# Performance work log

Hardware: AMD Instinct MI355X
Metric: run time of the kernel (lower is better)

## Reference

```python
import jax, jax.numpy as jnp
import numpy as np

N_NODES = 100000
N_EDGES = 3200000
IN_DIM = 128
OUT_DIM = 128


def setup_inputs() -> dict:
    key = jax.random.key(0)
    k1, k2, k3, k4, k5 = jax.random.split(key, 5)
    fea_input = jax.random.normal(k1, (N_NODES, IN_DIM), dtype=jnp.float32)
    edge_row = jax.random.randint(k2, (N_EDGES,), 0, N_NODES, dtype=jnp.int32)
    edge_col = jax.random.randint(k3, (N_EDGES,), 0, N_NODES, dtype=jnp.int32)
    edge_val = jax.random.uniform(k4, (N_EDGES,), dtype=jnp.float32)
    # kaiming_uniform-style init for weight, zeros for bias
    bound = float(np.sqrt(6.0 / IN_DIM))
    weight = jax.random.uniform(k5, (IN_DIM, OUT_DIM), dtype=jnp.float32,
                                minval=-bound, maxval=bound)
    bias = jnp.zeros((OUT_DIM,), dtype=jnp.float32)
    return {
        "fea_input": fea_input,
        "edge_row": edge_row,
        "edge_col": edge_col,
        "edge_val": edge_val,
        "weight": weight,
        "bias": bias,
    }


def reference(fea_input, edge_row, edge_col, edge_val, weight, bias):
    # support = X @ W  -> [N, OUT_DIM]
    support = jnp.matmul(fea_input, weight)
    # SpMM: out[r] += val * support[c] for each edge (r, c, val)
    gathered = support[edge_col] * edge_val[:, None]  # [E, OUT_DIM]
    output = jax.ops.segment_sum(gathered, edge_row, num_segments=N_NODES)
    return output + bias
```

## Files before the change

kernel.cpp:

```cpp
#include <hip/hip_runtime.h>
#include <hip/hip_bf16.h>


#define N_NODES 100000
#define N_EDGES 3200000
#define DIM 128
#define RB 16
#define RPB 64
#define NBKT ((N_NODES + RPB - 1) / RPB)
#define CHUNK 8192
#define NCHK ((N_EDGES + CHUNK - 1) / CHUNK)
#define CAP3 2688

typedef __attribute__((ext_vector_type(8))) short bf16x8;
typedef __attribute__((ext_vector_type(4))) float f32x4;
typedef unsigned long long u64;
typedef unsigned int u32;

__device__ inline ushort bf16rne(float f) {
  uint32_t u = __float_as_uint(f);
  u += 0x7fffu + ((u >> 16) & 1u);
  return (ushort)(u >> 16);
}
__device__ inline float lofl(u32 u) { return __uint_as_float(u << 16); }
__device__ inline float hifl(u32 u) { return __uint_as_float(u & 0xffff0000u); }

__global__ __launch_bounds__(256) void prep_count_kernel(
    const float* __restrict__ X, const float* __restrict__ W,
    ushort* __restrict__ Xh, ushort* __restrict__ Wh,
    const int* __restrict__ erow, int* __restrict__ bcnt,
    int* __restrict__ table) {
  __shared__ int cnt[NBKT];
  if (blockIdx.x < 1024) {
    const size_t nx4 = (size_t)N_NODES * DIM / 4;
    const size_t nw4 = (size_t)DIM * DIM / 4;
    for (size_t i = (size_t)blockIdx.x * blockDim.x + threadIdx.x;
         i < nx4 + nw4; i += (size_t)1024 * blockDim.x) {
      const float4 f = (i < nx4) ? ((const float4*)X)[i] : ((const float4*)W)[i - nx4];
      ushort4 h;
      h.x = bf16rne(f.x); h.y = bf16rne(f.y); h.z = bf16rne(f.z); h.w = bf16rne(f.w);
      if (i < nx4) ((ushort4*)Xh)[i] = h;
      else         ((ushort4*)Wh)[i - nx4] = h;
    }
  } else {
    const int cb = blockIdx.x - 1024;
    for (int b = threadIdx.x; b < NBKT; b += 256) cnt[b] = 0;
    __syncthreads();
    const int e0 = cb * CHUNK;
    #pragma unroll
    for (int it = 0; it < CHUNK / 256; ++it) {
      const int e = e0 + it * 256 + threadIdx.x;
      if (e < N_EDGES) atomicAdd(&cnt[erow[e] >> 6], 1);
    }
    __syncthreads();
    for (int b = threadIdx.x; b < NBKT; b += 256) {
      const int c = cnt[b];
      table[(size_t)cb * NBKT + b] = c;
      if (c) atomicAdd(&bcnt[b], c);
    }
  }
}

__global__ __launch_bounds__(1024) void bscan_kernel(int* __restrict__ bcur,
                                                     int* __restrict__ bbase) {
  __shared__ int wsum[32];
  const int t = threadIdx.x, lane = t & 63, wid = t >> 6;
  int v0 = (t < NBKT) ? bcur[t] : 0;
  int v1 = (t + 1024 < NBKT) ? bcur[t + 1024] : 0;
  int i0 = v0, i1 = v1;
  #pragma unroll
  for (int off = 1; off < 64; off <<= 1) {
    int n0 = __shfl_up(i0, off, 64);
    int n1 = __shfl_up(i1, off, 64);
    if (lane >= off) { i0 += n0; i1 += n1; }
  }
  if (lane == 63) { wsum[wid] = i0; wsum[16 + wid] = i1; }
  __syncthreads();
  if (t == 0) {
    int s = 0;
    #pragma unroll
    for (int k = 0; k < 32; ++k) { int x = wsum[k]; wsum[k] = s; s += x; }
    bbase[NBKT] = s;
  }
  __syncthreads();
  const int e0 = wsum[wid] + i0 - v0;
  const int e1 = wsum[16 + wid] + i1 - v1;
  if (t < NBKT) { bbase[t] = e0; bcur[t] = e0; }
  if (t + 1024 < NBKT) { bbase[t + 1024] = e1; bcur[t + 1024] = e1; }
}

__global__ __launch_bounds__(256) void partition_kernel(
    const int* __restrict__ erow, const int* __restrict__ ecol,
    const float* __restrict__ eval, const int* __restrict__ table,
    int* __restrict__ bcur, u64* __restrict__ p64) {
  __shared__ int cnt[NBKT];
  const int e0 = blockIdx.x * CHUNK;
  for (int b = threadIdx.x; b < NBKT; b += 256) {
    const int c = table[(size_t)blockIdx.x * NBKT + b];
    cnt[b] = c ? atomicAdd(&bcur[b], c) : 0;
  }
  __syncthreads();
  #pragma unroll
  for (int it = 0; it < CHUNK / 256; ++it) {
    const int e = e0 + it * 256 + threadIdx.x;
    if (e < N_EDGES) {
      const int r = erow[e];
      const u32 lo = ((u32)ecol[e] << 15) | (u32)bf16rne(eval[e]);
      const int p = atomicAdd(&cnt[r >> 6], 1);
      p64[p] = ((u64)(r & (RPB - 1)) << 32) | (u64)lo;
    }
  }
}

__global__ __launch_bounds__(256) void agg_sort_kernel(
    const ushort* __restrict__ Xh,
    const int* __restrict__ bbase, const u64* __restrict__ p64,
    ushort* __restrict__ Yh) {
  __shared__ u32 sbuf[CAP3];
  __shared__ int hist[RPB];
  __shared__ int rstart[RPB];
  __shared__ int curs[RPB];
  const int b = blockIdx.x, t = threadIdx.x;
  const int s = bbase[b];
  int nE = bbase[b + 1] - s;
  if (nE > CAP3) nE = CAP3;

  if (t < RPB) hist[t] = 0;
  __syncthreads();
  for (int i = t; i < nE; i += 256)
    atomicAdd(&hist[(int)(p64[s + i] >> 32) & (RPB - 1)], 1);
  __syncthreads();
  if (t < RPB) {
    const int v = hist[t];
    int incl = v;
    #pragma unroll
    for (int off = 1; off < 64; off <<= 1) {
      int n = __shfl_up(incl, off, 64);
      if (t >= off) incl += n;
    }
    rstart[t] = incl - v;
    curs[t] = incl - v;
  }
  __syncthreads();
  for (int i = t; i < nE; i += 256) {
    const u64 w = p64[s + i];
    const int p = atomicAdd(&curs[(int)(w >> 32) & (RPB - 1)], 1);
    sbuf[p] = (u32)w;
  }
  __syncthreads();

  const int wid = t >> 6, lane = t & 63;
  const int q = lane >> 4;
  const u32 sub16 = (u32)(lane & 15) * 16u;
  const char* Xb = (const char*)Xh;
  #pragma unroll 1
  for (int j = 0; j < 16; ++j) {
    const int rl = wid * 16 + j;
    const int gr = b * RPB + rl;
    const int s0 = rstart[rl];
    const int s1 = s0 + hist[rl];
    float f0 = 0.f, f1 = 0.f, f2 = 0.f, f3 = 0.f;
    float f4 = 0.f, f5 = 0.f, f6 = 0.f, f7 = 0.f;
    #pragma unroll 1
    for (int e = s0 + q; e < s1; e += 16) {
      const u32 lo0 = sbuf[e];
      const u32 lo1 = (e + 4  < s1) ? sbuf[e + 4]  : 0u;
      const u32 lo2 = (e + 8  < s1) ? sbuf[e + 8]  : 0u;
      const u32 lo3 = (e + 12 < s1) ? sbuf[e + 12] : 0u;
      const u32 o0 = (lo0 >> 7) & 0xFFFFFF00u;
      const u32 o1 = (lo1 >> 7) & 0xFFFFFF00u;
      const u32 o2 = (lo2 >> 7) & 0xFFFFFF00u;
      const u32 o3 = (lo3 >> 7) & 0xFFFFFF00u;
      const uint4 g0 = *(const uint4*)(Xb + (o0 + sub16));
      const uint4 g1 = *(const uint4*)(Xb + (o1 + sub16));
      const uint4 g2 = *(const uint4*)(Xb + (o2 + sub16));
      const uint4 g3 = *(const uint4*)(Xb + (o3 + sub16));
      const float v0 = __uint_as_float((lo0 & 0x7fffu) << 16);
      const float v1 = __uint_as_float((lo1 & 0x7fffu) << 16);
      const float v2 = __uint_as_float((lo2 & 0x7fffu) << 16);
      const float v3 = __uint_as_float((lo3 & 0x7fffu) << 16);
      f0 += v0 * lofl(g0.x); f1 += v0 * hifl(g0.x);
      f2 += v0 * lofl(g0.y); f3 += v0 * hifl(g0.y);
      f4 += v0 * lofl(g0.z); f5 += v0 * hifl(g0.z);
      f6 += v0 * lofl(g0.w); f7 += v0 * hifl(g0.w);
      f0 += v1 * lofl(g1.x); f1 += v1 * hifl(g1.x);
      f2 += v1 * lofl(g1.y); f3 += v1 * hifl(g1.y);
      f4 += v1 * lofl(g1.z); f5 += v1 * hifl(g1.z);
      f6 += v1 * lofl(g1.w); f7 += v1 * hifl(g1.w);
      f0 += v2 * lofl(g2.x); f1 += v2 * hifl(g2.x);
      f2 += v2 * lofl(g2.y); f3 += v2 * hifl(g2.y);
      f4 += v2 * lofl(g2.z); f5 += v2 * hifl(g2.z);
      f6 += v2 * lofl(g2.w); f7 += v2 * hifl(g2.w);
      f0 += v3 * lofl(g3.x); f1 += v3 * hifl(g3.x);
      f2 += v3 * lofl(g3.y); f3 += v3 * hifl(g3.y);
      f4 += v3 * lofl(g3.z); f5 += v3 * hifl(g3.z);
      f6 += v3 * lofl(g3.w); f7 += v3 * hifl(g3.w);
    }
    f0 += __shfl_xor(f0, 16); f1 += __shfl_xor(f1, 16);
    f2 += __shfl_xor(f2, 16); f3 += __shfl_xor(f3, 16);
    f4 += __shfl_xor(f4, 16); f5 += __shfl_xor(f5, 16);
    f6 += __shfl_xor(f6, 16); f7 += __shfl_xor(f7, 16);
    f0 += __shfl_xor(f0, 32); f1 += __shfl_xor(f1, 32);
    f2 += __shfl_xor(f2, 32); f3 += __shfl_xor(f3, 32);
    f4 += __shfl_xor(f4, 32); f5 += __shfl_xor(f5, 32);
    f6 += __shfl_xor(f6, 32); f7 += __shfl_xor(f7, 32);
    if (gr < N_NODES && lane < 16) {
      uint4 o;
      o.x = (u32)bf16rne(f0) | ((u32)bf16rne(f1) << 16);
      o.y = (u32)bf16rne(f2) | ((u32)bf16rne(f3) << 16);
      o.z = (u32)bf16rne(f4) | ((u32)bf16rne(f5) << 16);
      o.w = (u32)bf16rne(f6) | ((u32)bf16rne(f7) << 16);
      ((uint4*)(Yh + (size_t)gr * DIM))[lane] = o;
    }
  }
}

__global__ __launch_bounds__(256) void gemm_mfma(const ushort* __restrict__ Yh,
                                                 const ushort* __restrict__ Wh,
                                                 const float* __restrict__ bias,
                                                 float* __restrict__ out) {
  const int wid = threadIdx.x >> 6, lane = threadIdx.x & 63;
  const int lr = lane & 15, lq = lane >> 4;
  const int n0 = wid * 32;

  bf16x8 bfrag[4][2];
  float bval[2];
  #pragma unroll
  for (int nt = 0; nt < 2; ++nt) {
    const int col = n0 + nt * 16 + lr;
    bval[nt] = bias[col];
    #pragma unroll
    for (int kk = 0; kk < 4; ++kk) {
      const int kbase = kk * 32 + lq * 8;
      bf16x8 b;
      #pragma unroll
      for (int i = 0; i < 8; ++i)
        b[i] = (short)Wh[(size_t)(kbase + i) * DIM + col];
      bfrag[kk][nt] = b;
    }
  }

  const int r0 = blockIdx.x * 256;
  #pragma unroll 1
  for (int g = 0; g < 16; ++g) {
    const int m0 = r0 + g * 16;
    if (m0 >= N_NODES) break;
    bf16x8 afrag[4];
    const ushort* arow = Yh + (size_t)(m0 + lr) * DIM + lq * 8;
    #pragma unroll
    for (int kk = 0; kk < 4; ++kk)
      afrag[kk] = *(const bf16x8*)(arow + kk * 32);
    #pragma unroll
    for (int nt = 0; nt < 2; ++nt) {
      f32x4 acc = {0.f, 0.f, 0.f, 0.f};
      #pragma unroll
      for (int kk = 0; kk < 4; ++kk)
        acc = __builtin_amdgcn_mfma_f32_16x16x32_bf16(afrag[kk], bfrag[kk][nt], acc, 0, 0, 0);
      const int col = n0 + nt * 16 + lr;
      #pragma unroll
      for (int j = 0; j < 4; ++j)
        out[(size_t)(m0 + lq * 4 + j) * DIM + col] = acc[j] + bval[nt];
    }
  }
}

__global__ __launch_bounds__(128) void gemm_kernel(
    const float* __restrict__ IN, const float* __restrict__ W,
    float* __restrict__ OUT, const float* __restrict__ bias, int add_bias) {
  __shared__ float Wsh[DIM * DIM];
  __shared__ float Xsh[RB * DIM];
  const int t = threadIdx.x;
  #pragma unroll 8
  for (int i = 0; i < DIM; ++i) Wsh[i * DIM + t] = W[i * DIM + t];
  const int r0 = blockIdx.x * RB;
  #pragma unroll
  for (int idx = t; idx < RB * DIM; idx += 128)
    Xsh[idx] = IN[(size_t)r0 * DIM + idx];
  __syncthreads();
  float acc[RB];
  const float b = add_bias ? bias[t] : 0.f;
  #pragma unroll
  for (int r = 0; r < RB; ++r) acc[r] = b;
  for (int k = 0; k < DIM; ++k) {
    const float w = Wsh[k * DIM + t];
    #pragma unroll
    for (int r = 0; r < RB; ++r) acc[r] += Xsh[r * DIM + k] * w;
  }
  #pragma unroll
  for (int r = 0; r < RB; ++r)
    OUT[(size_t)(r0 + r) * DIM + t] = acc[r];
}

__global__ void init_kernel(float* __restrict__ out, const float* __restrict__ bias) {
  const size_t total4 = (size_t)N_NODES * DIM / 4;
  const float4* b4 = (const float4*)bias;
  float4* o4 = (float4*)out;
  for (size_t i = (size_t)blockIdx.x * blockDim.x + threadIdx.x;
       i < total4; i += (size_t)gridDim.x * blockDim.x)
    o4[i] = b4[i & 31];
}

__global__ __launch_bounds__(256) void scatter_kernel(
    const float* __restrict__ S,
    const int* __restrict__ erow, const int* __restrict__ ecol,
    const float* __restrict__ eval, float* __restrict__ out) {
  const long long g = (long long)blockIdx.x * blockDim.x + threadIdx.x;
  const long long e = g >> 5;
  const int lane = (int)(g & 31);
  if (e >= N_EDGES) return;
  const int r = erow[e];
  const int c = ecol[e];
  const float v = eval[e];
  const float4 x = ((const float4*)(S + (size_t)c * DIM))[lane];
  float* o = out + (size_t)r * DIM + lane * 4;
  atomicAdd(o + 0, v * x.x);
  atomicAdd(o + 1, v * x.y);
  atomicAdd(o + 2, v * x.z);
  atomicAdd(o + 3, v * x.w);
}

extern "C" void kernel_launch(void* const* d_in, const int* in_sizes, int n_in,
                              void* d_out, int out_size, void* d_ws, size_t ws_size,
                              hipStream_t stream) {
  const float* X    = (const float*)d_in[0];
  const int*   erow = (const int*)d_in[1];
  const int*   ecol = (const int*)d_in[2];
  const float* eval = (const float*)d_in[3];
  const float* W    = (const float*)d_in[4];
  const float* bias = (const float*)d_in[5];
  float* out = (float*)d_out;

  const size_t P64_BYTES = (size_t)N_EDGES * 8;
  const size_t XH_BYTES  = (size_t)N_NODES * DIM * 2;
  const size_t YH_BYTES  = (size_t)N_NODES * DIM * 2;
  const size_t WH_BYTES  = (size_t)DIM * DIM * 2;
  const size_t BB_BYTES  = (size_t)(NBKT + 1) * 4;
  const size_t BC_BYTES  = (size_t)NBKT * 4;
  const size_t NEED = P64_BYTES + XH_BYTES + YH_BYTES + WH_BYTES +
                      BB_BYTES + BC_BYTES + 256;

  if (ws_size >= NEED) {
    char* w = (char*)d_ws;
    u64*    p64     = (u64*)w;     w += P64_BYTES;
    ushort* Xh      = (ushort*)w;  w += XH_BYTES;
    ushort* Yh      = (ushort*)w;  w += YH_BYTES;
    ushort* Wh      = (ushort*)w;  w += WH_BYTES;
    int*    bbase   = (int*)w;     w += BB_BYTES;
    int*    bcur    = (int*)w;
    int*    table   = (int*)Yh;

    hipMemsetAsync(bcur, 0, BC_BYTES, stream);
    prep_count_kernel<<<1024 + NCHK, 256, 0, stream>>>(X, W, Xh, Wh, erow, bcur, table);
    bscan_kernel<<<1, 1024, 0, stream>>>(bcur, bbase);
    partition_kernel<<<NCHK, 256, 0, stream>>>(erow, ecol, eval, table, bcur, p64);
    agg_sort_kernel<<<NBKT, 256, 0, stream>>>(Xh, bbase, p64, Yh);
    gemm_mfma<<<(N_NODES + 255) / 256, 256, 0, stream>>>(Yh, Wh, bias, out);
  } else {
    float* S = (float*)d_ws;
    init_kernel<<<2048, 256, 0, stream>>>(out, bias);
    gemm_kernel<<<N_NODES / RB, 128, 0, stream>>>(X, W, S, bias, 0);
    const long long threads = (long long)N_EDGES * 32;
    scatter_kernel<<<(int)((threads + 255) / 256), 256, 0, stream>>>(S, erow, ecol, eval, out);
  }
}
```

Measured before the change: 232.4 us.

## Replace atomic bucket offsets with per-bucket chunk prefix scan; pre-transpose W

Bucket offsets are no longer claimed with global atomics. Per-chunk histograms are exclusive-scanned per bucket in a new column-scan kernel, so each partition block gets deterministic write offsets, and the memset goes away. Separately, W is stored transposed in bf16 so the GEMM loads each B fragment with one vector load instead of eight strided scalar loads. The cost is an extra kernel launch and a strided scan over the table, where each lane reads a value NBKT ints apart.

```diff
diff --git a/kernel.cpp b/kernel.cpp
--- a/kernel.cpp
+++ b/kernel.cpp
@@ -27,20 +27,28 @@
 
 __global__ __launch_bounds__(256) void prep_count_kernel(
     const float* __restrict__ X, const float* __restrict__ W,
-    ushort* __restrict__ Xh, ushort* __restrict__ Wh,
-    const int* __restrict__ erow, int* __restrict__ bcnt,
-    int* __restrict__ table) {
+    ushort* __restrict__ Xh, ushort* __restrict__ WhT,
+    const int* __restrict__ erow, int* __restrict__ table) {
   __shared__ int cnt[NBKT];
   if (blockIdx.x < 1024) {
     const size_t nx4 = (size_t)N_NODES * DIM / 4;
     const size_t nw4 = (size_t)DIM * DIM / 4;
     for (size_t i = (size_t)blockIdx.x * blockDim.x + threadIdx.x;
          i < nx4 + nw4; i += (size_t)1024 * blockDim.x) {
-      const float4 f = (i < nx4) ? ((const float4*)X)[i] : ((const float4*)W)[i - nx4];
-      ushort4 h;
-      h.x = bf16rne(f.x); h.y = bf16rne(f.y); h.z = bf16rne(f.z); h.w = bf16rne(f.w);
-      if (i < nx4) ((ushort4*)Xh)[i] = h;
-      else         ((ushort4*)Wh)[i - nx4] = h;
+      if (i < nx4) {
+        const float4 f = ((const float4*)X)[i];
+        ushort4 h;
+        h.x = bf16rne(f.x); h.y = bf16rne(f.y); h.z = bf16rne(f.z); h.w = bf16rne(f.w);
+        ((ushort4*)Xh)[i] = h;
+      } else {
+        const float4 f = ((const float4*)W)[i - nx4];
+        const int elem = (int)(i - nx4) * 4;
+        const int k = elem >> 7, col = elem & 127;
+        WhT[(size_t)(col + 0) * DIM + k] = bf16rne(f.x);
+        WhT[(size_t)(col + 1) * DIM + k] = bf16rne(f.y);
+        WhT[(size_t)(col + 2) * DIM + k] = bf16rne(f.z);
+        WhT[(size_t)(col + 3) * DIM + k] = bf16rne(f.w);
+      }
     }
   } else {
     const int cb = blockIdx.x - 1024;
@@ -53,20 +61,39 @@
       if (e < N_EDGES) atomicAdd(&cnt[erow[e] >> 6], 1);
     }
     __syncthreads();
-    for (int b = threadIdx.x; b < NBKT; b += 256) {
-      const int c = cnt[b];
-      table[(size_t)cb * NBKT + b] = c;
-      if (c) atomicAdd(&bcnt[b], c);
-    }
-  }
-}
-
-__global__ __launch_bounds__(1024) void bscan_kernel(int* __restrict__ bcur,
+    for (int b = threadIdx.x; b < NBKT; b += 256)
+      table[(size_t)cb * NBKT + b] = cnt[b];
+  }
+}
+
+__global__ __launch_bounds__(256) void cscan_kernel(int* __restrict__ table,
+                                                    int* __restrict__ bcnt) {
+  const int b = blockIdx.x * 4 + (threadIdx.x >> 6);
+  if (b >= NBKT) return;
+  const int lane = threadIdx.x & 63;
+  int carry = 0;
+  #pragma unroll
+  for (int r = 0; r < (NCHK + 63) / 64; ++r) {
+    const int cb = r * 64 + lane;
+    const int c = (cb < NCHK) ? table[(size_t)cb * NBKT + b] : 0;
+    int incl = c;
+    #pragma unroll
+    for (int off = 1; off < 64; off <<= 1) {
+      int n = __shfl_up(incl, off, 64);
+      if (lane >= off) incl += n;
+    }
+    if (cb < NCHK) table[(size_t)cb * NBKT + b] = carry + incl - c;
+    carry += __shfl(incl, 63, 64);
+  }
+  if (lane == 0) bcnt[b] = carry;
+}
+
+__global__ __launch_bounds__(1024) void bscan_kernel(const int* __restrict__ bcnt,
                                                      int* __restrict__ bbase) {
   __shared__ int wsum[32];
   const int t = threadIdx.x, lane = t & 63, wid = t >> 6;
-  int v0 = (t < NBKT) ? bcur[t] : 0;
-  int v1 = (t + 1024 < NBKT) ? bcur[t + 1024] : 0;
+  int v0 = (t < NBKT) ? bcnt[t] : 0;
+  int v1 = (t + 1024 < NBKT) ? bcnt[t + 1024] : 0;
   int i0 = v0, i1 = v1;
   #pragma unroll
   for (int off = 1; off < 64; off <<= 1) {
@@ -83,22 +110,18 @@
     bbase[NBKT] = s;
   }
   __syncthreads();
-  const int e0 = wsum[wid] + i0 - v0;
-  const int e1 = wsum[16 + wid] + i1 - v1;
-  if (t < NBKT) { bbase[t] = e0; bcur[t] = e0; }
-  if (t + 1024 < NBKT) { bbase[t + 1024] = e1; bcur[t + 1024] = e1; }
+  if (t < NBKT) bbase[t] = wsum[wid] + i0 - v0;
+  if (t + 1024 < NBKT) bbase[t + 1024] = wsum[16 + wid] + i1 - v1;
 }
 
 __global__ __launch_bounds__(256) void partition_kernel(
     const int* __restrict__ erow, const int* __restrict__ ecol,
     const float* __restrict__ eval, const int* __restrict__ table,
-    int* __restrict__ bcur, u64* __restrict__ p64) {
+    const int* __restrict__ bbase, u64* __restrict__ p64) {
   __shared__ int cnt[NBKT];
   const int e0 = blockIdx.x * CHUNK;
-  for (int b = threadIdx.x; b < NBKT; b += 256) {
-    const int c = table[(size_t)blockIdx.x * NBKT + b];
-    cnt[b] = c ? atomicAdd(&bcur[b], c) : 0;
-  }
+  for (int b = threadIdx.x; b < NBKT; b += 256)
+    cnt[b] = bbase[b] + table[(size_t)blockIdx.x * NBKT + b];
   __syncthreads();
   #pragma unroll
   for (int it = 0; it < CHUNK / 256; ++it) {
@@ -216,7 +239,7 @@
 }
 
 __global__ __launch_bounds__(256) void gemm_mfma(const ushort* __restrict__ Yh,
-                                                 const ushort* __restrict__ Wh,
+                                                 const ushort* __restrict__ WhT,
                                                  const float* __restrict__ bias,
                                                  float* __restrict__ out) {
   const int wid = threadIdx.x >> 6, lane = threadIdx.x & 63;
@@ -230,14 +253,8 @@
     const int col = n0 + nt * 16 + lr;
     bval[nt] = bias[col];
     #pragma unroll
-    for (int kk = 0; kk < 4; ++kk) {
-      const int kbase = kk * 32 + lq * 8;
-      bf16x8 b;
-      #pragma unroll
-      for (int i = 0; i < 8; ++i)
-        b[i] = (short)Wh[(size_t)(kbase + i) * DIM + col];
-      bfrag[kk][nt] = b;
-    }
+    for (int kk = 0; kk < 4; ++kk)
+      bfrag[kk][nt] = *(const bf16x8*)(WhT + (size_t)col * DIM + kk * 32 + lq * 8);
   }
 
   const int r0 = blockIdx.x * 256;
@@ -333,10 +350,10 @@
   const size_t P64_BYTES = (size_t)N_EDGES * 8;
   const size_t XH_BYTES  = (size_t)N_NODES * DIM * 2;
   const size_t YH_BYTES  = (size_t)N_NODES * DIM * 2;
-  const size_t WH_BYTES  = (size_t)DIM * DIM * 2;
+  const size_t WHT_BYTES = (size_t)DIM * DIM * 2;
   const size_t BB_BYTES  = (size_t)(NBKT + 1) * 4;
   const size_t BC_BYTES  = (size_t)NBKT * 4;
-  const size_t NEED = P64_BYTES + XH_BYTES + YH_BYTES + WH_BYTES +
+  const size_t NEED = P64_BYTES + XH_BYTES + YH_BYTES + WHT_BYTES +
                       BB_BYTES + BC_BYTES + 256;
 
   if (ws_size >= NEED) {
@@ -344,17 +361,17 @@
     u64*    p64     = (u64*)w;     w += P64_BYTES;
     ushort* Xh      = (ushort*)w;  w += XH_BYTES;
     ushort* Yh      = (ushort*)w;  w += YH_BYTES;
-    ushort* Wh      = (ushort*)w;  w += WH_BYTES;
+    ushort* WhT     = (ushort*)w;  w += WHT_BYTES;
     int*    bbase   = (int*)w;     w += BB_BYTES;
-    int*    bcur    = (int*)w;
+    int*    bcnt    = (int*)w;     w += BC_BYTES;
     int*    table   = (int*)Yh;
 
-    hipMemsetAsync(bcur, 0, BC_BYTES, stream);
-    prep_count_kernel<<<1024 + NCHK, 256, 0, stream>>>(X, W, Xh, Wh, erow, bcur, table);
-    bscan_kernel<<<1, 1024, 0, stream>>>(bcur, bbase);
-    partition_kernel<<<NCHK, 256, 0, stream>>>(erow, ecol, eval, table, bcur, p64);
+    prep_count_kernel<<<1024 + NCHK, 256, 0, stream>>>(X, W, Xh, WhT, erow, table);
+    cscan_kernel<<<(NBKT + 3) / 4, 256, 0, stream>>>(table, bcnt);
+    bscan_kernel<<<1, 1024, 0, stream>>>(bcnt, bbase);
+    partition_kernel<<<NCHK, 256, 0, stream>>>(erow, ecol, eval, table, bbase, p64);
     agg_sort_kernel<<<NBKT, 256, 0, stream>>>(Xh, bbase, p64, Yh);
-    gemm_mfma<<<(N_NODES + 255) / 256, 256, 0, stream>>>(Yh, Wh, bias, out);
+    gemm_mfma<<<(N_NODES + 255) / 256, 256, 0, stream>>>(Yh, WhT, bias, out);
   } else {
     float* S = (float*)d_ws;
     init_kernel<<<2048, 256, 0, stream>>>(out, bias);
```

New measurement: 210.9 us. 9.2% less time.
